# Kernel optimization log

Hardware: AMD Instinct MI355X
Metric: run time of the kernel (lower is better)

## Reference

```python
import jax, jax.numpy as jnp
import numpy as np

IN_FEATURES = 1024
OUT_FEATURES = 1024
GRID_SIZE = 5
SPLINE_ORDER = 3
GRID_RANGE = (-1.0, 1.0)


def make_grid():
    h = (GRID_RANGE[1] - GRID_RANGE[0]) / GRID_SIZE
    g = jnp.arange(-SPLINE_ORDER, GRID_SIZE + SPLINE_ORDER + 1, dtype=jnp.float32) * h + GRID_RANGE[0]
    return jnp.tile(g[None, :], (IN_FEATURES, 1))  # (in, G + 2k + 1)


def b_splines(x, grid):
    # x: (N, in), grid: (in, G+2k+1) -> bases: (N, in, G+k)
    xe = x[..., None]
    bases = ((xe >= grid[:, :-1]) & (xe < grid[:, 1:])).astype(x.dtype)
    for k in range(1, SPLINE_ORDER + 1):
        left = (xe - grid[:, :-(k + 1)]) / (grid[:, k:-1] - grid[:, :-(k + 1)])
        right = (grid[:, k + 1:] - xe) / (grid[:, k + 1:] - grid[:, 1:-k])
        bases = left * bases[:, :, :-1] + right * bases[:, :, 1:]
    return bases


def setup_inputs() -> dict:
    key = jax.random.key(0)
    k1, k2, k3 = jax.random.split(key, 3)
    x = jax.random.uniform(k1, (8192, IN_FEATURES), dtype=jnp.float32)
    # lecun_normal-style init: std = 1/sqrt(fan_in)
    base_weight = jax.random.normal(k2, (OUT_FEATURES, IN_FEATURES), dtype=jnp.float32) / np.sqrt(IN_FEATURES)
    coeff = GRID_SIZE + SPLINE_ORDER
    spline_weight = jax.random.normal(k3, (OUT_FEATURES, IN_FEATURES, coeff), dtype=jnp.float32) / np.sqrt(IN_FEATURES * coeff)
    spline_scaler = jnp.ones((OUT_FEATURES, IN_FEATURES), dtype=jnp.float32)
    grid = make_grid()
    return {"x": x, "grid": grid, "base_weight": base_weight,
            "spline_weight": spline_weight, "spline_scaler": spline_scaler}


def reference(x, grid, base_weight, spline_weight, spline_scaler):
    N = x.shape[0]
    base_out = jax.nn.silu(x) @ base_weight.T  # (N, out)
    bases = b_splines(x, grid)                 # (N, in, G+k)
    scaled_sw = spline_weight * spline_scaler[..., None]  # (out, in, G+k)
    spline_out = bases.reshape(N, -1) @ scaled_sw.reshape(OUT_FEATURES, -1).T  # (N, out)
    return base_out + spline_out
```

## Files before the change

### kernel.cpp

```cpp
#include <hip/hip_runtime.h>
#include <hip/hip_bf16.h>

#define IN_F 1024
#define OUT_F 1024
#define KTOT (IN_F * 9)
#define M_ROWS 8192

#define BM 256
#define BN 128
#define BK 64
#define NT (KTOT / BK)

typedef short bf16x8 __attribute__((ext_vector_type(8)));
typedef int   i32x4  __attribute__((ext_vector_type(4)));
typedef float f32x4  __attribute__((ext_vector_type(4)));

#define AS1 __attribute__((address_space(1)))
#define AS3 __attribute__((address_space(3)))

__device__ __forceinline__ void kan_basis_fast(
    float xv, const float* __restrict__ g,
    const float* __restrict__ inv1, const float* __restrict__ inv2,
    const float* __restrict__ inv3, float* __restrict__ out) {
  float b[11];
#pragma unroll
  for (int j = 0; j < 11; ++j)
    b[j] = (xv >= g[j] && xv < g[j + 1]) ? 1.0f : 0.0f;
#pragma unroll
  for (int j = 0; j < 10; ++j)
    b[j] = (xv - g[j]) * inv1[j] * b[j] + (g[j + 2] - xv) * inv1[j + 1] * b[j + 1];
#pragma unroll
  for (int j = 0; j < 9; ++j)
    b[j] = (xv - g[j]) * inv2[j] * b[j] + (g[j + 3] - xv) * inv2[j + 1] * b[j + 1];
#pragma unroll
  for (int j = 0; j < 8; ++j)
    b[j] = (xv - g[j]) * inv3[j] * b[j] + (g[j + 4] - xv) * inv3[j + 1] * b[j + 1];
#pragma unroll
  for (int j = 0; j < 8; ++j) out[j] = b[j];
}

__global__ __launch_bounds__(256) void expand_a(
    const float* __restrict__ x, const float* __restrict__ grid,
    __hip_bfloat16* __restrict__ A, int row0, int nrows) {
  int t = blockIdx.x * 256 + threadIdx.x;
  int n = t >> 7;
  if (n >= nrows) return;
  int i0 = (t & 127) * 8;

  float g[12];
  const float* gp = grid + (size_t)i0 * 12;
#pragma unroll
  for (int j = 0; j < 12; ++j) g[j] = gp[j];
  float inv1[11], inv2[10], inv3[9];
#pragma unroll
  for (int j = 0; j < 11; ++j) inv1[j] = 1.0f / (g[j + 1] - g[j]);
#pragma unroll
  for (int j = 0; j < 10; ++j) inv2[j] = 1.0f / (g[j + 2] - g[j]);
#pragma unroll
  for (int j = 0; j < 9; ++j)  inv3[j] = 1.0f / (g[j + 3] - g[j]);

  const float* xp = x + (size_t)(row0 + n) * IN_F + i0;
  float xs[8];
  *(f32x4*)&xs[0] = *(const f32x4*)xp;
  *(f32x4*)&xs[4] = *(const f32x4*)(xp + 4);

  bf16x8 out[9];
#pragma unroll
  for (int j = 0; j < 8; ++j) {
    float xv = xs[j];
    float bas[8];
    kan_basis_fast(xv, g, inv1, inv2, inv3, bas);
    float s = xv / (1.0f + __expf(-xv));
    out[0][j] = (short)__bfloat16_as_ushort(__float2bfloat16(s));
#pragma unroll
    for (int c = 0; c < 8; ++c)
      out[c + 1][j] = (short)__bfloat16_as_ushort(__float2bfloat16(bas[c]));
  }
  __hip_bfloat16* dst = A + (size_t)n * KTOT + i0;
#pragma unroll
  for (int c = 0; c < 9; ++c)
    *(bf16x8*)(dst + (size_t)c * IN_F) = out[c];
}

__global__ __launch_bounds__(256) void pack_b(
    const float* __restrict__ bw, const float* __restrict__ sw,
    const float* __restrict__ sc, __hip_bfloat16* __restrict__ B) {
  int t = blockIdx.x * 256 + threadIdx.x;
  if (t >= OUT_F * 128) return;
  int o = t >> 7;
  int i0 = (t & 127) * 8;

  float bwv[8], scv[8];
  const float* bp = bw + (size_t)o * IN_F + i0;
  const float* sp = sc + (size_t)o * IN_F + i0;
  *(f32x4*)&bwv[0] = *(const f32x4*)bp;
  *(f32x4*)&bwv[4] = *(const f32x4*)(bp + 4);
  *(f32x4*)&scv[0] = *(const f32x4*)sp;
  *(f32x4*)&scv[4] = *(const f32x4*)(sp + 4);

  bf16x8 out[9];
#pragma unroll
  for (int j = 0; j < 8; ++j) {
    out[0][j] = (short)__bfloat16_as_ushort(__float2bfloat16(bwv[j]));
    const float* swp = sw + ((size_t)o * IN_F + i0 + j) * 8;
    float swv[8];
    *(f32x4*)&swv[0] = *(const f32x4*)swp;
    *(f32x4*)&swv[4] = *(const f32x4*)(swp + 4);
#pragma unroll
    for (int c = 0; c < 8; ++c)
      out[c + 1][j] = (short)__bfloat16_as_ushort(__float2bfloat16(swv[c] * scv[j]));
  }
  __hip_bfloat16* dst = B + (size_t)o * KTOT + i0;
#pragma unroll
  for (int c = 0; c < 9; ++c)
    *(bf16x8*)(dst + (size_t)c * IN_F) = out[c];
}


__device__ __forceinline__ void gld16(const __hip_bfloat16* g, __hip_bfloat16* l) {
  __builtin_amdgcn_global_load_lds((AS1 void*)g, (AS3 void*)l, 16, 0, 0);
}

__device__ __forceinline__ bf16x8 dsr128(uint32_t addr) {
  i32x4 r;
  asm volatile("ds_read_b128 %0, %1" : "=v"(r) : "v"(addr));
  return __builtin_bit_cast(bf16x8, r);
}

#define MFMA16(d, a, b) d = __builtin_amdgcn_mfma_f32_16x16x32_bf16(a, b, d, 0, 0, 0)

#define DO_PHASE(kk, STAGE, TAIL) do {                                    \
    bf16x8 a0 = dsr128(aS + aOffB[kk][0]);                                \
    bf16x8 a1 = dsr128(aS + aOffB[kk][1]);                                \
    bf16x8 a2 = dsr128(aS + aOffB[kk][2]);                                \
    bf16x8 a3 = dsr128(aS + aOffB[kk][3]);                                \
    bf16x8 b0 = dsr128(bS + bOffB[kk][0]);                                \
    bf16x8 b1 = dsr128(bS + bOffB[kk][1]);                                \
    bf16x8 b2 = dsr128(bS + bOffB[kk][2]);                                \
    bf16x8 b3 = dsr128(bS + bOffB[kk][3]);                                \
    STAGE                                                                 \
    __builtin_amdgcn_sched_barrier(0);                                    \
    __builtin_amdgcn_s_barrier();                                         \
    asm volatile("s_waitcnt lgkmcnt(0)" ::: "memory");                    \
    __builtin_amdgcn_sched_barrier(0);                                    \
    __builtin_amdgcn_s_setprio(1);                                        \
    MFMA16(acc[0][0], a0, b0); MFMA16(acc[0][1], a0, b1);                 \
    MFMA16(acc[0][2], a0, b2); MFMA16(acc[0][3], a0, b3);                 \
    MFMA16(acc[1][0], a1, b0); MFMA16(acc[1][1], a1, b1);                 \
    MFMA16(acc[1][2], a1, b2); MFMA16(acc[1][3], a1, b3);                 \
    MFMA16(acc[2][0], a2, b0); MFMA16(acc[2][1], a2, b1);                 \
    MFMA16(acc[2][2], a2, b2); MFMA16(acc[2][3], a2, b3);                 \
    MFMA16(acc[3][0], a3, b0); MFMA16(acc[3][1], a3, b1);                 \
    MFMA16(acc[3][2], a3, b2); MFMA16(acc[3][3], a3, b3);                 \
    __builtin_amdgcn_s_setprio(0);                                        \
    __builtin_amdgcn_sched_barrier(0);                                    \
    TAIL                                                                  \
    __builtin_amdgcn_s_barrier();                                         \
    __builtin_amdgcn_sched_barrier(0);                                    \
  } while (0)

__global__ __launch_bounds__(512, 2) void gemm_v4(
    const __hip_bfloat16* __restrict__ A, const __hip_bfloat16* __restrict__ B,
    float* __restrict__ C) {
  __shared__ __align__(16) __hip_bfloat16 As[3][BM * BK];
  __shared__ __align__(16) __hip_bfloat16 Bs[3][BN * BK];

  const int nwg = gridDim.x;
  const int q = nwg >> 3;
  const int L = (blockIdx.x & 7) * q + (blockIdx.x >> 3);
  const int bm = L >> 3, bn = L & 7;

  const int tid = threadIdx.x;
  const int lane = tid & 63;
  const int wv = tid >> 6;
  const int wm = wv >> 1;
  const int wn = wv & 1;
  const int l15 = lane & 15, lhi = lane >> 4;
  const int K = KTOT;

  const __hip_bfloat16* aSrc[4];
  const __hip_bfloat16* bSrc[2];
  int aDst[4], bDst[2];
#pragma unroll
  for (int j = 0; j < 4; ++j) {
    int p = j * 512 + wv * 64 + lane;
    int row = p >> 3;
    int col = (p & 7) ^ (row & 7);
    aSrc[j] = A + (size_t)(bm * BM + row) * K + col * 8;
    aDst[j] = (j * 512 + wv * 64) * 8;
  }
#pragma unroll
  for (int j = 0; j < 2; ++j) {
    int p = j * 512 + wv * 64 + lane;
    int row = p >> 3;
    int col = (p & 7) ^ (row & 7);
    bSrc[j] = B + (size_t)(bn * BN + row) * K + col * 8;
    bDst[j] = (j * 512 + wv * 64) * 8;
  }

  const uint32_t aBase = (uint32_t)(uintptr_t)(AS3 const void*)&As[0][0];
  const uint32_t bBase = (uint32_t)(uintptr_t)(AS3 const void*)&Bs[0][0];
  uint32_t aOffB[2][4], bOffB[2][4];
#pragma unroll
  for (int kk = 0; kk < 2; ++kk)
#pragma unroll
    for (int m = 0; m < 4; ++m) {
      int rowA = wm * 64 + m * 16 + l15;
      aOffB[kk][m] = (rowA * 64 + (((kk * 4 + lhi) ^ (l15 & 7)) * 8)) * 2;
      int rowB = wn * 64 + m * 16 + l15;
      bOffB[kk][m] = (rowB * 64 + (((kk * 4 + lhi) ^ (l15 & 7)) * 8)) * 2;
    }

  f32x4 acc[4][4];
#pragma unroll
  for (int m = 0; m < 4; ++m)
#pragma unroll
    for (int n = 0; n < 4; ++n) acc[m][n] = f32x4{0.f, 0.f, 0.f, 0.f};

#pragma unroll
  for (int j = 0; j < 4; ++j) gld16(aSrc[j], &As[0][0] + aDst[j]);
#pragma unroll
  for (int j = 0; j < 2; ++j) gld16(bSrc[j], &Bs[0][0] + bDst[j]);
#pragma unroll
  for (int j = 0; j < 4; ++j) gld16(aSrc[j] + BK, &As[1][0] + aDst[j]);
#pragma unroll
  for (int j = 0; j < 2; ++j) gld16(bSrc[j] + BK, &Bs[1][0] + bDst[j]);
  asm volatile("s_waitcnt vmcnt(6)" ::: "memory");
  __builtin_amdgcn_s_barrier();

  int cur = 0, stg = 2;
  for (int t = 0; t < NT - 2; ++t) {
    const uint32_t aS = aBase + (uint32_t)cur * (BM * BK * 2);
    const uint32_t bS = bBase + (uint32_t)cur * (BN * BK * 2);
    __hip_bfloat16* asD = &As[stg][0];
    __hip_bfloat16* bsD = &Bs[stg][0];
    const int kt2 = (t + 2) * BK;

    DO_PHASE(0,
      { gld16(aSrc[0] + kt2, asD + aDst[0]);
        gld16(aSrc[1] + kt2, asD + aDst[1]);
        gld16(aSrc[2] + kt2, asD + aDst[2]); },
      {});
    DO_PHASE(1,
      { gld16(aSrc[3] + kt2, asD + aDst[3]);
        gld16(bSrc[0] + kt2, bsD + bDst[0]);
        gld16(bSrc[1] + kt2, bsD + bDst[1]); },
      { asm volatile("s_waitcnt vmcnt(6)" ::: "memory"); });

    cur = cur == 2 ? 0 : cur + 1;
    stg = stg == 2 ? 0 : stg + 1;
  }
  {
    const uint32_t aS = aBase + (uint32_t)cur * (BM * BK * 2);
    const uint32_t bS = bBase + (uint32_t)cur * (BN * BK * 2);
    DO_PHASE(0, {}, {});
    DO_PHASE(1, {}, { asm volatile("s_waitcnt vmcnt(0)" ::: "memory"); });
    cur = cur == 2 ? 0 : cur + 1;
  }
  {
    const uint32_t aS = aBase + (uint32_t)cur * (BM * BK * 2);
    const uint32_t bS = bBase + (uint32_t)cur * (BN * BK * 2);
    DO_PHASE(0, {}, {});
    DO_PHASE(1, {}, {});
  }

#pragma unroll
  for (int m = 0; m < 4; ++m)
#pragma unroll
    for (int n = 0; n < 4; ++n) {
      int col = bn * BN + wn * 64 + n * 16 + l15;
      int row0 = bm * BM + wm * 64 + m * 16 + lhi * 4;
#pragma unroll
      for (int j = 0; j < 4; ++j)
        C[(size_t)(row0 + j) * OUT_F + col] = acc[m][n][j];
    }
}

__global__ __launch_bounds__(256) void kan_naive(
    const float* __restrict__ x, const float* __restrict__ grid,
    const float* __restrict__ bw, const float* __restrict__ sw,
    const float* __restrict__ sc, float* __restrict__ out) {
  __shared__ float s_act[IN_F];
  __shared__ float s_bas[IN_F * 8];
  int n = blockIdx.x;
  for (int i = threadIdx.x; i < IN_F; i += 256) {
    float xv = x[(size_t)n * IN_F + i];
    float g[12];
    const float* gp = grid + i * 12;
#pragma unroll
    for (int t = 0; t < 12; ++t) g[t] = gp[t];
    float b[11];
#pragma unroll
    for (int j = 0; j < 11; ++j)
      b[j] = (xv >= g[j] && xv < g[j + 1]) ? 1.0f : 0.0f;
#pragma unroll
    for (int k = 1; k <= 3; ++k)
#pragma unroll
      for (int j = 0; j < 11 - k; ++j) {
        float left = (xv - g[j]) / (g[j + k] - g[j]);
        float right = (g[j + k + 1] - xv) / (g[j + k + 1] - g[j + 1]);
        b[j] = left * b[j] + right * b[j + 1];
      }
    s_act[i] = xv / (1.0f + __expf(-xv));
#pragma unroll
    for (int c = 0; c < 8; ++c) s_bas[i * 8 + c] = b[c];
  }
  __syncthreads();
  for (int o = threadIdx.x; o < OUT_F; o += 256) {
    float acc = 0.f;
    const float* bwo = bw + (size_t)o * IN_F;
    const float* swo = sw + (size_t)o * IN_F * 8;
    const float* sco = sc + (size_t)o * IN_F;
    for (int i = 0; i < IN_F; ++i) {
      acc += s_act[i] * bwo[i];
      float p = 0.f;
#pragma unroll
      for (int c = 0; c < 8; ++c) p += s_bas[i * 8 + c] * swo[i * 8 + c];
      acc += p * sco[i];
    }
    out[(size_t)n * OUT_F + o] = acc;
  }
}

extern "C" void kernel_launch(void* const* d_in, const int* in_sizes, int n_in,
                              void* d_out, int out_size, void* d_ws, size_t ws_size,
                              hipStream_t stream) {
  const float* x  = (const float*)d_in[0];
  const float* grid = (const float*)d_in[1];
  const float* bw = (const float*)d_in[2];
  const float* sw = (const float*)d_in[3];
  const float* sc = (const float*)d_in[4];
  float* out = (float*)d_out;

  const size_t Bbytes = (size_t)OUT_F * KTOT * 2;
  const size_t rowBytes = (size_t)KTOT * 2;

  if (ws_size >= Bbytes + 256 * rowBytes) {
    __hip_bfloat16* Bp = (__hip_bfloat16*)d_ws;
    __hip_bfloat16* Ap = (__hip_bfloat16*)((char*)d_ws + Bbytes);
    size_t arows = (ws_size - Bbytes) / rowBytes;
    int chunk = (int)((arows / 256) * 256);
    if (chunk > M_ROWS) chunk = M_ROWS;

    pack_b<<<OUT_F * 128 / 256, 256, 0, stream>>>(bw, sw, sc, Bp);
    for (int r0 = 0; r0 < M_ROWS; r0 += chunk) {
      int rows = M_ROWS - r0 < chunk ? M_ROWS - r0 : chunk;
      expand_a<<<(rows * 128 + 255) / 256, 256, 0, stream>>>(x, grid, Ap, r0, rows);
      gemm_v4<<<(rows / BM) * 8, 512, 0, stream>>>(Ap, Bp, out + (size_t)r0 * OUT_F);
    }
  } else {
    kan_naive<<<M_ROWS, 256, 0, stream>>>(x, grid, bw, sw, sc, out);
  }
}
```

Before: 196.1 us.

## Merge two K-phases into one barrier per tile with split LDS waits

Restructures the GEMM main loop so each BK tile uses a single workgroup barrier instead of two. All LDS fragment reads for both k-halves are issued up front, and partial lgkmcnt waits let the first 16 MFMAs start while the second half's reads are still in flight. The global prefetch of the next tile is issued in one group. This removes barrier overhead and exposes more LDS-read overlap, but it doubles the live fragment registers, which could raise register pressure at 2 waves per SIMD.

```diff
diff --git a/kernel.cpp b/kernel.cpp
--- a/kernel.cpp
+++ b/kernel.cpp
@@ -129,19 +129,32 @@
 
 #define MFMA16(d, a, b) d = __builtin_amdgcn_mfma_f32_16x16x32_bf16(a, b, d, 0, 0, 0)
 
-#define DO_PHASE(kk, STAGE, TAIL) do {                                    \
-    bf16x8 a0 = dsr128(aS + aOffB[kk][0]);                                \
-    bf16x8 a1 = dsr128(aS + aOffB[kk][1]);                                \
-    bf16x8 a2 = dsr128(aS + aOffB[kk][2]);                                \
-    bf16x8 a3 = dsr128(aS + aOffB[kk][3]);                                \
-    bf16x8 b0 = dsr128(bS + bOffB[kk][0]);                                \
-    bf16x8 b1 = dsr128(bS + bOffB[kk][1]);                                \
-    bf16x8 b2 = dsr128(bS + bOffB[kk][2]);                                \
-    bf16x8 b3 = dsr128(bS + bOffB[kk][3]);                                \
+#define DO_TILE(VMN, STAGE) do {                                          \
+    const uint32_t aS = aBase + (uint32_t)cur * (BM * BK * 2);            \
+    const uint32_t bS = bBase + (uint32_t)cur * (BN * BK * 2);            \
+    asm volatile("s_waitcnt vmcnt(" #VMN ")" ::: "memory");               \
+    __builtin_amdgcn_sched_barrier(0);                                    \
+    __builtin_amdgcn_s_barrier();                                         \
+    __builtin_amdgcn_sched_barrier(0);                                    \
+    bf16x8 a0 = dsr128(aS + aOffB[0][0]);                                 \
+    bf16x8 a1 = dsr128(aS + aOffB[0][1]);                                 \
+    bf16x8 a2 = dsr128(aS + aOffB[0][2]);                                 \
+    bf16x8 a3 = dsr128(aS + aOffB[0][3]);                                 \
+    bf16x8 b0 = dsr128(bS + bOffB[0][0]);                                 \
+    bf16x8 b1 = dsr128(bS + bOffB[0][1]);                                 \
+    bf16x8 b2 = dsr128(bS + bOffB[0][2]);                                 \
+    bf16x8 b3 = dsr128(bS + bOffB[0][3]);                                 \
+    bf16x8 a4 = dsr128(aS + aOffB[1][0]);                                 \
+    bf16x8 a5 = dsr128(aS + aOffB[1][1]);                                 \
+    bf16x8 a6 = dsr128(aS + aOffB[1][2]);                                 \
+    bf16x8 a7 = dsr128(aS + aOffB[1][3]);                                 \
+    bf16x8 b4 = dsr128(bS + bOffB[1][0]);                                 \
+    bf16x8 b5 = dsr128(bS + bOffB[1][1]);                                 \
+    bf16x8 b6 = dsr128(bS + bOffB[1][2]);                                 \
+    bf16x8 b7 = dsr128(bS + bOffB[1][3]);                                 \
     STAGE                                                                 \
     __builtin_amdgcn_sched_barrier(0);                                    \
-    __builtin_amdgcn_s_barrier();                                         \
-    asm volatile("s_waitcnt lgkmcnt(0)" ::: "memory");                    \
+    asm volatile("s_waitcnt lgkmcnt(8)" ::: "memory");                    \
     __builtin_amdgcn_sched_barrier(0);                                    \
     __builtin_amdgcn_s_setprio(1);                                        \
     MFMA16(acc[0][0], a0, b0); MFMA16(acc[0][1], a0, b1);                 \
@@ -154,12 +167,22 @@
     MFMA16(acc[3][2], a3, b2); MFMA16(acc[3][3], a3, b3);                 \
     __builtin_amdgcn_s_setprio(0);                                        \
     __builtin_amdgcn_sched_barrier(0);                                    \
-    TAIL                                                                  \
-    __builtin_amdgcn_s_barrier();                                         \
+    asm volatile("s_waitcnt lgkmcnt(0)" ::: "memory");                    \
+    __builtin_amdgcn_sched_barrier(0);                                    \
+    __builtin_amdgcn_s_setprio(1);                                        \
+    MFMA16(acc[0][0], a4, b4); MFMA16(acc[0][1], a4, b5);                 \
+    MFMA16(acc[0][2], a4, b6); MFMA16(acc[0][3], a4, b7);                 \
+    MFMA16(acc[1][0], a5, b4); MFMA16(acc[1][1], a5, b5);                 \
+    MFMA16(acc[1][2], a5, b6); MFMA16(acc[1][3], a5, b7);                 \
+    MFMA16(acc[2][0], a6, b4); MFMA16(acc[2][1], a6, b5);                 \
+    MFMA16(acc[2][2], a6, b6); MFMA16(acc[2][3], a6, b7);                 \
+    MFMA16(acc[3][0], a7, b4); MFMA16(acc[3][1], a7, b5);                 \
+    MFMA16(acc[3][2], a7, b6); MFMA16(acc[3][3], a7, b7);                 \
+    __builtin_amdgcn_s_setprio(0);                                        \
     __builtin_amdgcn_sched_barrier(0);                                    \
   } while (0)
 
-__global__ __launch_bounds__(512, 2) void gemm_v4(
+__global__ __launch_bounds__(512, 2) void gemm_v5(
     const __hip_bfloat16* __restrict__ A, const __hip_bfloat16* __restrict__ B,
     float* __restrict__ C) {
   __shared__ __align__(16) __hip_bfloat16 As[3][BM * BK];
@@ -225,44 +248,25 @@
   for (int j = 0; j < 4; ++j) gld16(aSrc[j] + BK, &As[1][0] + aDst[j]);
 #pragma unroll
   for (int j = 0; j < 2; ++j) gld16(bSrc[j] + BK, &Bs[1][0] + bDst[j]);
-  asm volatile("s_waitcnt vmcnt(6)" ::: "memory");
-  __builtin_amdgcn_s_barrier();
 
   int cur = 0, stg = 2;
   for (int t = 0; t < NT - 2; ++t) {
-    const uint32_t aS = aBase + (uint32_t)cur * (BM * BK * 2);
-    const uint32_t bS = bBase + (uint32_t)cur * (BN * BK * 2);
     __hip_bfloat16* asD = &As[stg][0];
     __hip_bfloat16* bsD = &Bs[stg][0];
     const int kt2 = (t + 2) * BK;
-
-    DO_PHASE(0,
+    DO_TILE(6,
       { gld16(aSrc[0] + kt2, asD + aDst[0]);
         gld16(aSrc[1] + kt2, asD + aDst[1]);
-        gld16(aSrc[2] + kt2, asD + aDst[2]); },
-      {});
-    DO_PHASE(1,
-      { gld16(aSrc[3] + kt2, asD + aDst[3]);
+        gld16(aSrc[2] + kt2, asD + aDst[2]);
+        gld16(aSrc[3] + kt2, asD + aDst[3]);
         gld16(bSrc[0] + kt2, bsD + bDst[0]);
-        gld16(bSrc[1] + kt2, bsD + bDst[1]); },
-      { asm volatile("s_waitcnt vmcnt(6)" ::: "memory"); });
-
+        gld16(bSrc[1] + kt2, bsD + bDst[1]); });
     cur = cur == 2 ? 0 : cur + 1;
     stg = stg == 2 ? 0 : stg + 1;
   }
-  {
-    const uint32_t aS = aBase + (uint32_t)cur * (BM * BK * 2);
-    const uint32_t bS = bBase + (uint32_t)cur * (BN * BK * 2);
-    DO_PHASE(0, {}, {});
-    DO_PHASE(1, {}, { asm volatile("s_waitcnt vmcnt(0)" ::: "memory"); });
-    cur = cur == 2 ? 0 : cur + 1;
-  }
-  {
-    const uint32_t aS = aBase + (uint32_t)cur * (BM * BK * 2);
-    const uint32_t bS = bBase + (uint32_t)cur * (BN * BK * 2);
-    DO_PHASE(0, {}, {});
-    DO_PHASE(1, {}, {});
-  }
+  DO_TILE(6, {});
+  cur = cur == 2 ? 0 : cur + 1;
+  DO_TILE(0, {});
 
 #pragma unroll
   for (int m = 0; m < 4; ++m)
@@ -346,7 +350,7 @@
     for (int r0 = 0; r0 < M_ROWS; r0 += chunk) {
       int rows = M_ROWS - r0 < chunk ? M_ROWS - r0 : chunk;
       expand_a<<<(rows * 128 + 255) / 256, 256, 0, stream>>>(x, grid, Ap, r0, rows);
-      gemm_v4<<<(rows / BM) * 8, 512, 0, stream>>>(Ap, Bp, out + (size_t)r0 * OUT_F);
+      gemm_v5<<<(rows / BM) * 8, 512, 0, stream>>>(Ap, Bp, out + (size_t)r0 * OUT_F);
     }
   } else {
     kan_naive<<<M_ROWS, 256, 0, stream>>>(x, grid, bw, sw, sc, out);
```

New measurement: 188.9 us. -3.7%, faster.
